# Kernel optimization log

Hardware: AMD Instinct MI355X
Metric: run time of the kernel (lower is better)

Reference implementation:

```python
import jax, jax.numpy as jnp
import numpy as np
import math

N = 4096      # nodes
E = 131072    # edges (avg degree 32)
C = 128       # input channels
RATIO = 0.5   # TopKPooling default ratio
DIMS = [(128, 256), (256, 512), (512, 512), (512, 256), (256, 128)]


def setup_inputs() -> dict:
    key = jax.random.key(0)
    ks = jax.random.split(key, 16)
    inp = {}
    inp['x'] = jax.random.normal(ks[0], (N, C), jnp.float32)
    inp['edge_index'] = jax.random.randint(ks[1], (2, E), 0, N, jnp.int32)
    for i, (fi, fo) in enumerate(DIMS):
        inp[f'w{i}'] = jax.random.normal(ks[2 + i], (fi, fo), jnp.float32) / np.sqrt(fi).astype(np.float32)
        inp[f'b{i}'] = jnp.zeros((fo,), jnp.float32)
    inp['p0'] = jax.random.normal(ks[10], (256,), jnp.float32)
    inp['p1'] = jax.random.normal(ks[11], (512,), jnp.float32)
    return inp


def _gcn(x, M, w, b):
    # GCNConv: add self loops (weight 1), symmetric D^-1/2 normalization with
    # deg computed over target (col) index, aggregate messages src->dst.
    # M[r, c] = weight of edge (src=r, dst=c); dense equivalent of sparse conv.
    n = M.shape[0]
    Mc = M + jnp.eye(n, dtype=M.dtype)
    deg = Mc.sum(axis=0)
    dis = jnp.where(deg > 0, jax.lax.rsqrt(deg), 0.0)
    A = dis[:, None] * Mc * dis[None, :]          # normalized (src, dst)
    return jax.nn.relu(A.T @ (x @ w) + b)          # out[dst] = sum_src A * xW


def _augment(M):
    # augment_adj: add self loops then spspmm(A, A) -> dense (M+I) @ (M+I)
    B = M + jnp.eye(M.shape[0], dtype=M.dtype)
    return B @ B


def _pool(x, M, p):
    # TopKPooling: score = tanh(x.p / ||p||), keep top ceil(ratio*n) nodes,
    # gate kept features by score, slice adjacency to kept nodes.
    s = jnp.tanh((x @ p) / jnp.linalg.norm(p))
    k = int(math.ceil(RATIO * x.shape[0]))
    vals, perm = jax.lax.top_k(s, k)
    return x[perm] * vals[:, None], M[perm][:, perm], perm


def reference(x, edge_index, w0, b0, w1, b1, w2, b2, w3, b3, w4, b4, p0, p1):
    # dense adjacency M[src, dst] from edge list with unit edge weights
    M = jnp.zeros((N, N), jnp.float32).at[edge_index[0], edge_index[1]].add(1.0)

    # down block 0
    x = _gcn(x, M, w0, b0)
    res0, M0 = x, M
    x, M, perm0 = _pool(x, _augment(M), p0)

    # down block 1
    x = _gcn(x, M, w1, b1)
    res1, M1 = x, M
    x, M, perm1 = _pool(x, _augment(M), p1)

    # bottleneck
    x = _gcn(x, M, w2, b2)

    # up block 1: scatter into zeros, sum residual
    up = jnp.zeros_like(res1).at[perm1].set(x)
    x = _gcn(res1 + up, M1, w3, b3)

    # up block 0
    up = jnp.zeros_like(res0).at[perm0].set(x)
    x = _gcn(res0 + up, M0, w4, b4)
    return x
```

## Files before the change

### kernel.cpp

```cpp
#include <hip/hip_runtime.h>

#define NN 4096
#define EE 131072
#define NP1 2048
#define NP2 1024

typedef __attribute__((ext_vector_type(8))) __bf16 bf16x8;
typedef __attribute__((ext_vector_type(4))) float f32x4;
typedef __attribute__((ext_vector_type(8))) unsigned short ushort8;

static __device__ inline unsigned short bfbits(__bf16 b) {
  union { __bf16 x; unsigned short u; } c; c.x = b; return c.u;
}
static __device__ inline void split2(float v, unsigned short& h, unsigned short& l) {
  __bf16 hb = (__bf16)v;
  float hf = (float)hb;
  __bf16 lb = (__bf16)(v - hf);
  h = bfbits(hb); l = bfbits(lb);
}

static __device__ inline size_t pchunk(int r, int k, int NT) {
  return ((size_t)(r >> 4) * NT + (k >> 5)) * 64 + (((k >> 3) & 3) << 4) + (r & 15);
}


__global__ void hist_kernel(const int* __restrict__ src, const int* __restrict__ dst,
                            int* __restrict__ cnt_src, int* __restrict__ cnt_dst, int E) {
  int e = blockIdx.x * blockDim.x + threadIdx.x;
  if (e < E) {
    atomicAdd(&cnt_src[src[e]], 1);
    atomicAdd(&cnt_dst[dst[e]], 1);
  }
}

__global__ __launch_bounds__(1024) void scan2(const int* __restrict__ cnt_dst,
                                              const int* __restrict__ cnt_src,
                                              int* __restrict__ csc_off, int* __restrict__ csr_off,
                                              float* __restrict__ dis0, int n) {
  __shared__ int tmp[4096];
  const int* in = blockIdx.x ? cnt_src : cnt_dst;
  int* out = blockIdx.x ? csr_off : csc_off;
  int tid = threadIdx.x;
  for (int i = tid; i < n; i += 1024) {
    int v = in[i];
    tmp[i] = v;
    if (blockIdx.x == 0) dis0[i] = rsqrtf((float)v + 1.0f);
  }
  __syncthreads();
  for (int off = 1; off < n; off <<= 1) {
    int v[4];
    int c = 0;
    for (int i = tid; i < n; i += 1024) { v[c++] = (i >= off) ? tmp[i - off] : 0; }
    __syncthreads();
    c = 0;
    for (int i = tid; i < n; i += 1024) { tmp[i] += v[c++]; }
    __syncthreads();
  }
  for (int i = tid; i < n; i += 1024) out[i + 1] = tmp[i];
  if (tid == 0) out[0] = 0;
}

__global__ void scatter_kernel(const int* __restrict__ src, const int* __restrict__ dst,
                               const int* __restrict__ csc_off, const int* __restrict__ csr_off,
                               int* __restrict__ fill_dst, int* __restrict__ fill_src,
                               int* __restrict__ csc_src, int* __restrict__ csr_dst, int E) {
  int e = blockIdx.x * blockDim.x + threadIdx.x;
  if (e < E) {
    int s = src[e], d = dst[e];
    int p = atomicAdd(&fill_dst[d], 1);
    csc_src[csc_off[d] + p] = s;
    int q = atomicAdd(&fill_src[s], 1);
    csr_dst[csr_off[s] + q] = d;
  }
}

__global__ void pnorm2(const float* __restrict__ p0, const float* __restrict__ p1,
                       float* __restrict__ outv) {
  const float* p = blockIdx.x ? p1 : p0;
  int C = blockIdx.x ? 512 : 256;
  int tid = threadIdx.x;
  float acc = 0.f;
  for (int j = tid; j < C; j += 256) { float v = p[j]; acc += v * v; }
  for (int o = 32; o > 0; o >>= 1) acc += __shfl_down(acc, o);
  __shared__ float red[4];
  if ((tid & 63) == 0) red[tid >> 6] = acc;
  __syncthreads();
  if (tid == 0) outv[blockIdx.x] = sqrtf(red[0] + red[1] + red[2] + red[3]);
}


__global__ void score_key(const float* __restrict__ X, const float* __restrict__ p,
                          const float* __restrict__ pn, float* __restrict__ s,
                          unsigned long long* __restrict__ keys, int C) {
  int i = blockIdx.x;
  int tid = threadIdx.x;
  float acc = 0.f;
  for (int j = tid; j < C; j += 256) acc += X[(size_t)i * C + j] * p[j];
  for (int o = 32; o > 0; o >>= 1) acc += __shfl_down(acc, o);
  __shared__ float red[4];
  if ((tid & 63) == 0) red[tid >> 6] = acc;
  __syncthreads();
  if (tid == 0) {
    float sv = tanhf((red[0] + red[1] + red[2] + red[3]) / pn[0]);
    s[i] = sv;
    unsigned u = __float_as_uint(sv);
    unsigned m = (u & 0x80000000u) ? ~u : (u | 0x80000000u);
    keys[i] = (((unsigned long long)(~m)) << 32) | (unsigned)i;
  }
}

__global__ __launch_bounds__(256) void rank_count(const unsigned long long* __restrict__ keys,
                                                  int* __restrict__ rank) {
  __shared__ unsigned long long kk[512];
  int tid = threadIdx.x;
  int cand = blockIdx.x * 256 + tid;
  int base = blockIdx.y * 512;
  kk[tid] = keys[base + tid];
  kk[tid + 256] = keys[base + tid + 256];
  __syncthreads();
  unsigned long long kc = keys[cand];
  int c = 0;
#pragma unroll 8
  for (int t = 0; t < 512; ++t) c += (kk[t] < kc) ? 1 : 0;
  atomicAdd(&rank[cand], c);
}

__global__ void rank_place(const float* __restrict__ s, const int* __restrict__ rank, int k, int n,
                           int* __restrict__ kept, int* __restrict__ perm, float* __restrict__ vals,
                           int* __restrict__ cntk) {
  int i = blockIdx.x * blockDim.x + threadIdx.x;
  if (i < n) {
    int r = rank[i];
    int isk = (r < k) ? 1 : 0;
    if (isk) { perm[r] = i; vals[r] = s[i]; kept[i] = r; }
    else kept[i] = -1;
    if (cntk) cntk[i] = isk;
  }
}

__global__ void pool_gather_s(const float* __restrict__ X, const int* __restrict__ perm,
                              const float* __restrict__ vals, const float* __restrict__ dis,
                              float* __restrict__ out, int C) {
  int a = blockIdx.x;
  int r = perm[a];
  float v = vals[a] * dis[a];
  for (int j = threadIdx.x; j < C; j += blockDim.x)
    out[(size_t)a * C + j] = X[(size_t)r * C + j] * v;
}

__global__ void pool_split_p(const float* __restrict__ X, const int* __restrict__ perm,
                             const float* __restrict__ vals, unsigned short* __restrict__ h,
                             unsigned short* __restrict__ l, int C) {
  int a = blockIdx.x;
  int r = perm[a];
  float v = vals[a];
  int NT = C >> 5;
  for (int j0 = threadIdx.x * 8; j0 < C; j0 += 64 * 8) {
    ushort8 hv, lv;
#pragma unroll
    for (int e = 0; e < 8; ++e) {
      unsigned short he, le;
      split2(X[(size_t)r * C + j0 + e] * v, he, le);
      hv[e] = he; lv[e] = le;
    }
    size_t c = pchunk(a, j0, NT);
    *(ushort8*)&h[c * 8] = hv;
    *(ushort8*)&l[c * 8] = lv;
  }
}


__global__ __launch_bounds__(256) void aug_row_p(const int* __restrict__ csr_off,
                                                 const int* __restrict__ csr_dst,
                                                 const int* __restrict__ kept,
                                                 const int* __restrict__ perm,
                                                 unsigned short* __restrict__ rm) {
  __shared__ float acc[NP1];
  int ki = blockIdx.x;
  int r = perm[ki];
  for (int t = threadIdx.x; t < NP1; t += 256) acc[t] = 0.f;
  __syncthreads();
  int s = csr_off[r], e = csr_off[r + 1];
  int nm = e - s;
  int wave = threadIdx.x >> 6, lane = threadIdx.x & 63;
  for (int m = wave; m <= nm; m += 4) {
    int k = (m < nm) ? csr_dst[s + m] : r;
    int s2 = csr_off[k], e2 = csr_off[k + 1];
    int n2 = e2 - s2;
    for (int t = lane; t <= n2; t += 64) {
      int j = (t < n2) ? csr_dst[s2 + t] : k;
      int kj = kept[j];
      if (kj >= 0) atomicAdd(&acc[kj], 1.0f);
    }
  }
  __syncthreads();
  if (threadIdx.x == 0) acc[ki] += 1.0f;
  __syncthreads();
  int tid = threadIdx.x;
  ushort8 hv;
#pragma unroll
  for (int e8 = 0; e8 < 8; ++e8) hv[e8] = bfbits((__bf16)acc[tid * 8 + e8]);
  size_t dst = (((size_t)(ki >> 4)) * 64 + (tid >> 2)) * 64 + (size_t)(tid & 3) * 16 + (ki & 15);
  *(ushort8*)&rm[dst * 8] = hv;
}

__global__ void cnt_edges(const int* __restrict__ src, const int* __restrict__ dst,
                          const int* __restrict__ kept, int* __restrict__ cntk, int E) {
  int e = blockIdx.x * blockDim.x + threadIdx.x;
  if (e < E && kept[src[e]] >= 0) atomicAdd(&cntk[dst[e]], 1);
}

__global__ __launch_bounds__(256) void deg_gather(const int* __restrict__ csc_off,
                                                  const int* __restrict__ csc_src,
                                                  const int* __restrict__ cntk,
                                                  const int* __restrict__ perm,
                                                  float* __restrict__ dis) {
  int wid = threadIdx.x >> 6, lane = threadIdx.x & 63;
  int c = blockIdx.x * 4 + wid;
  int r = perm[c];
  int s = csc_off[r], e = csc_off[r + 1];
  int sum = 0;
  for (int t = s + lane; t < e; t += 64) sum += cntk[csc_src[t]];
  for (int o = 32; o > 0; o >>= 1) sum += __shfl_down(sum, o);
  if (lane == 0) dis[c] = rsqrtf((float)(sum + cntk[r] + 1));
}

__global__ __launch_bounds__(256) void t_pack(const unsigned short* __restrict__ in,
                                              unsigned short* __restrict__ outp, int n) {
  __shared__ unsigned short t[64][72];
  int r0 = blockIdx.y * 64, c0 = blockIdx.x * 64;
  int NT = n >> 5;
  for (int q = threadIdx.x; q < 512; q += 256) {
    int lt = q >> 6, l = q & 63;
    int rt = lt >> 1, kt2 = lt & 1;
    int r = rt * 16 + (l & 15), k = kt2 * 32 + (l >> 4) * 8;
    ushort8 v = *(const ushort8*)&in[pchunk(r0 + r, c0 + k, NT) * 8];
    *(ushort8*)&t[r][k] = v;
  }
  __syncthreads();
  for (int q = threadIdx.x; q < 512; q += 256) {
    int lt = q >> 6, l = q & 63;
    int jt = lt >> 1, kt2 = lt & 1;
    int j = jt * 16 + (l & 15), k = kt2 * 32 + (l >> 4) * 8;
    ushort8 v;
#pragma unroll
    for (int e = 0; e < 8; ++e) v[e] = t[k + e][j];
    *(ushort8*)&outp[pchunk(c0 + j, r0 + k, NT) * 8] = v;
  }
}

__global__ void dis_from_deg(const float* __restrict__ deg, float* __restrict__ dis, int n) {
  int i = blockIdx.x * blockDim.x + threadIdx.x;
  if (i < n) dis[i] = rsqrtf(deg[i]);
}


__global__ void split_p(const float* __restrict__ in, unsigned short* __restrict__ h,
                        unsigned short* __restrict__ l, int K) {
  int c = blockIdx.x * blockDim.x + threadIdx.x;
  int lane = c & 63, tile = c >> 6;
  int NT = K >> 5;
  int kt = tile % NT, rt = tile / NT;
  int r = rt * 16 + (lane & 15);
  int k = kt * 32 + (lane >> 4) * 8;
  const float* p = in + (size_t)r * K + k;
  ushort8 hv, lv;
#pragma unroll
  for (int e = 0; e < 8; ++e) {
    unsigned short he, le;
    split2(p[e], he, le);
    hv[e] = he; lv[e] = le;
  }
  *(ushort8*)&h[(size_t)c * 8] = hv;
  *(ushort8*)&l[(size_t)c * 8] = lv;
}

static __device__ inline void tsplit_body(const float* in, unsigned short* oh, unsigned short* ol,
                                          int R, int C, int c) {
  int lane = c & 63, tile = c >> 6;
  int NT = R >> 5;
  int kt = tile % NT, jt = tile / NT;
  int j = jt * 16 + (lane & 15);
  int k = kt * 32 + (lane >> 4) * 8;
  ushort8 hv, lv;
#pragma unroll
  for (int e = 0; e < 8; ++e) {
    unsigned short he, le;
    split2(in[(size_t)(k + e) * C + j], he, le);
    hv[e] = he; lv[e] = le;
  }
  *(ushort8*)&oh[(size_t)c * 8] = hv;
  *(ushort8*)&ol[(size_t)c * 8] = lv;
}

__global__ void tsplit_p(const float* __restrict__ in, unsigned short* __restrict__ oh,
                         unsigned short* __restrict__ ol, int R, int C) {
  int c = blockIdx.x * blockDim.x + threadIdx.x;
  tsplit_body(in, oh, ol, R, C, c);
}

__global__ void wconv_all(const float* w0, const float* w1, const float* w2,
                          const float* w3, const float* w4,
                          unsigned short* o0h, unsigned short* o0l,
                          unsigned short* o1h, unsigned short* o1l,
                          unsigned short* o2h, unsigned short* o2l,
                          unsigned short* o3h, unsigned short* o3l,
                          unsigned short* o4h, unsigned short* o4l) {
  int g = blockIdx.x * blockDim.x + threadIdx.x;
  if (g < 4096)        tsplit_body(w0, o0h, o0l, 128, 256, g);
  else if (g < 20480)  tsplit_body(w1, o1h, o1l, 256, 512, g - 4096);
  else if (g < 53248)  tsplit_body(w2, o2h, o2l, 512, 512, g - 20480);
  else if (g < 69632)  tsplit_body(w3, o3h, o3l, 512, 256, g - 53248);
  else                 tsplit_body(w4, o4h, o4l, 256, 128, g - 69632);
}

__global__ void gather2_p(const unsigned short* __restrict__ in0, const unsigned short* __restrict__ in1,
                          const int* __restrict__ perm,
                          unsigned short* __restrict__ out0, unsigned short* __restrict__ out1, int NT) {
  const unsigned short* in = blockIdx.y ? in1 : in0;
  unsigned short* outp = blockIdx.y ? out1 : out0;
  int c = blockIdx.x * blockDim.x + threadIdx.x;
  int lane = c & 63, tile = c >> 6;
  int kt = tile % NT, at = tile / NT;
  int a = at * 16 + (lane & 15);
  int sub = lane >> 4;
  int p = perm[a];
  size_t sc = ((size_t)(p >> 4) * NT + kt) * 64 + sub * 16 + (p & 15);
  *(ushort8*)&outp[(size_t)c * 8] = *(const ushort8*)&in[sc * 8];
}

__global__ void unpool_split_p(const float* __restrict__ res, const float* __restrict__ up,
                               const int* __restrict__ kept, unsigned short* __restrict__ h,
                               unsigned short* __restrict__ l, int C) {
  int c = blockIdx.x * blockDim.x + threadIdx.x;
  int lane = c & 63, tile = c >> 6;
  int NT = C >> 5;
  int kt = tile % NT, rt = tile / NT;
  int r = rt * 16 + (lane & 15);
  int j0 = kt * 32 + (lane >> 4) * 8;
  int kv = kept[r];
  ushort8 hv, lv;
#pragma unroll
  for (int e = 0; e < 8; ++e) {
    float v = res[(size_t)r * C + j0 + e];
    if (kv >= 0) v += up[(size_t)kv * C + j0 + e];
    unsigned short he, le;
// ... 31 lines not shown
  float* o = out + (size_t)c * C + j;
#pragma unroll
  for (int u = 0; u < VEC; ++u) o[u] = dc * acc[u];
}

template <int C>
__global__ __launch_bounds__(256) void spmm_gather_v(const float* __restrict__ Y,
                                                     const int* __restrict__ off,
                                                     const int* __restrict__ srcs,
                                                     const float* __restrict__ dis,
                                                     const float* __restrict__ bias,
                                                     float* __restrict__ out) {
  constexpr int VEC = C / 64;
  int w = threadIdx.x >> 6, lane = threadIdx.x & 63;
  int c = blockIdx.x * 4 + w;
  int j = lane * VEC;
  float acc[VEC];
  const float* p = Y + (size_t)c * C + j;
#pragma unroll
  for (int u = 0; u < VEC; ++u) acc[u] = p[u];
  int s = off[c], e = off[c + 1];
  for (int t = s; t < e; ++t) {
    const float* q = Y + (size_t)srcs[t] * C + j;
#pragma unroll
    for (int u = 0; u < VEC; ++u) acc[u] += q[u];
  }
  float d = dis[c];
  float* o = out + (size_t)c * C + j;
#pragma unroll
  for (int u = 0; u < VEC; ++u) o[u] = fmaxf(d * acc[u] + bias[j + u], 0.0f);
}


template <int S>
__global__ void ep3(const float* __restrict__ p, const float* __restrict__ rs,
                    const float* __restrict__ bias, float* __restrict__ outp, int M, int N) {
  int idx = blockIdx.x * blockDim.x + threadIdx.x;
  int j4 = (idx * 4) % N, i = (idx * 4) / N;
  float4 a = {0.f, 0.f, 0.f, 0.f};
#pragma unroll
  for (int s = 0; s < S; ++s) {
    float4 b = *(const float4*)(p + ((size_t)s * M + i) * N + j4);
    a.x += b.x; a.y += b.y; a.z += b.z; a.w += b.w;
  }
  float r = rs[i];
  float4 o;
  o.x = fmaxf(r * a.x + bias[j4 + 0], 0.f);
  o.y = fmaxf(r * a.y + bias[j4 + 1], 0.f);
  o.z = fmaxf(r * a.z + bias[j4 + 2], 0.f);
  o.w = fmaxf(r * a.w + bias[j4 + 3], 0.f);
  *(float4*)(outp + (size_t)i * N + j4) = o;
}

template <int S>
__global__ void ep_zsplit(const float* __restrict__ p, unsigned short* __restrict__ h,
                          unsigned short* __restrict__ l, int M, int N) {
  int t = blockIdx.x * blockDim.x + threadIdx.x;
  int tile = t >> 6, w = t & 63;
  int NT = N >> 5;
  int rt = tile / NT, kt = tile % NT;
  int r = rt * 16 + (w & 15);
  int k = kt * 32 + (w >> 4) * 8;
  const float* p0 = p + (size_t)r * N + k;
  ushort8 hv, lv;
#pragma unroll
  for (int e = 0; e < 8; ++e) {
    float v = p0[e];
#pragma unroll
    for (int s = 1; s < S; ++s) v += p0[(size_t)s * M * N + e];
    unsigned short he, le;
    split2(v, he, le);
    hv[e] = he; lv[e] = le;
  }
  *(ushort8*)&h[(size_t)t * 8] = hv;
  *(ushort8*)&l[(size_t)t * 8] = lv;
}

template <int S>
__global__ void ep_aug_cs(const float* __restrict__ p, float* __restrict__ B,
                          float* __restrict__ deg, int n) {
  int c = blockIdx.x * 256 + threadIdx.x;
  int r0 = blockIdx.y * 64;
  float cs = 0.f;
  for (int r = r0; r < r0 + 64; ++r) {
    float v = 0.f;
#pragma unroll
    for (int s = 0; s < S; ++s) v += p[((size_t)s * n + r) * n + c];
    if (r == c) v += 1.0f;
    B[(size_t)r * n + c] = v;
    cs += v;
  }
  atomicAdd(&deg[c], cs);
}

template <int EPI, int AL, int BL, int KK, int S>
__global__ __launch_bounds__(256) void gemm16(
    const unsigned short* __restrict__ Ah, const unsigned short* __restrict__ Al,
    const unsigned short* __restrict__ Bh, const unsigned short* __restrict__ Bl,
    int M, int N, const float* __restrict__ rs, const float* __restrict__ bias,
    float* __restrict__ C, unsigned short* __restrict__ Th, unsigned short* __restrict__ Tl) {
  static_assert(KK % 32 == 0, "K");
  constexpr int KSTEPS = KK / 32;
  const int NT = (KK * S) >> 5;
  const int gx = gridDim.x;
  int id = blockIdx.y * gx + blockIdx.x;
  int cpx = (gx * gridDim.y) >> 3;
  int sid = (id & 7) * cpx + (id >> 3);
  const int bx = sid % gx, by = sid / gx;
  const int z = (S > 1) ? blockIdx.z : 0;
  const int wid = threadIdx.x >> 6, lane = threadIdx.x & 63;
  const int i0 = by * 64 + (wid >> 1) * 32;
  const int j0 = bx * 64 + (wid & 1) * 32;
  const int lr = lane & 15, lk = lane >> 4;
  size_t aoff[2], boff[2];
#pragma unroll
  for (int t = 0; t < 2; ++t) {
    aoff[t] = ((size_t)((i0 >> 4) + t) * NT + z * (KK >> 5)) * 512 + lane * 8;
    boff[t] = ((size_t)((j0 >> 4) + t) * NT + z * (KK >> 5)) * 512 + lane * 8;
  }
  const f32x4 zf = {0.f, 0.f, 0.f, 0.f};
  f32x4 acc[2][2];
  acc[0][0] = zf; acc[0][1] = zf; acc[1][0] = zf; acc[1][1] = zf;

  bf16x8 ahf[4][2], bhf[4][2], alf[4][2], blf[4][2];
  auto loadk = [&](int kk, int b) {
    size_t o = (size_t)kk * 512;
    ahf[b][0] = *(const bf16x8*)(Ah + aoff[0] + o);
    ahf[b][1] = *(const bf16x8*)(Ah + aoff[1] + o);
// ... 16 lines not shown
        acc[am][bn] = __builtin_amdgcn_mfma_f32_16x16x32_bf16(ahf[b][am], bhf[b][bn], acc[am][bn], 0, 0, 0);
        if constexpr (BL)
          acc[am][bn] = __builtin_amdgcn_mfma_f32_16x16x32_bf16(ahf[b][am], blf[b][bn], acc[am][bn], 0, 0, 0);
        if constexpr (AL)
          acc[am][bn] = __builtin_amdgcn_mfma_f32_16x16x32_bf16(alf[b][am], bhf[b][bn], acc[am][bn], 0, 0, 0);
      }
  };

  loadk(0, 0);
  if constexpr (KSTEPS > 1) loadk(1, 1);
  if constexpr (KSTEPS > 2) loadk(2, 2);
#pragma unroll
  for (int kk = 0; kk < KSTEPS; ++kk) {
    const int cur = kk & 3;
    if (kk + 3 < KSTEPS) loadk(kk + 3, (cur + 3) & 3);
    domm(cur);
  }

#pragma unroll
  for (int am = 0; am < 2; ++am)
#pragma unroll
    for (int bn = 0; bn < 2; ++bn) {
      int ib = i0 + 16 * am + lk * 4;
      int j = j0 + 16 * bn + lr;
      f32x4 a = acc[am][bn];
      if constexpr (S > 1) {
#pragma unroll
        for (int r = 0; r < 4; ++r) C[((size_t)z * M + ib + r) * N + j] = a[r];
      } else if constexpr (EPI == 0) {
#pragma unroll
        for (int r = 0; r < 4; ++r) C[(size_t)(ib + r) * N + j] = a[r];
      } else if constexpr (EPI == 1) {
#pragma unroll
        for (int r = 0; r < 4; ++r) C[(size_t)(ib + r) * N + j] = rs[ib + r] * a[r];
      } else if constexpr (EPI == 2) {
        unsigned long long hp = 0, lp = 0;
#pragma unroll
        for (int r = 0; r < 4; ++r) {
          unsigned short hv, lv;
          split2(rs[ib + r] * a[r], hv, lv);
          hp |= ((unsigned long long)hv) << (16 * r);
          lp |= ((unsigned long long)lv) << (16 * r);
        }
        size_t c = pchunk(j, ib, M >> 5);
        *(unsigned long long*)&Th[c * 8 + (ib & 7)] = hp;
        *(unsigned long long*)&Tl[c * 8 + (ib & 7)] = lp;
      } else if constexpr (EPI == 3) {
#pragma unroll
        for (int r = 0; r < 4; ++r)
          C[(size_t)(ib + r) * N + j] = fmaxf(rs[ib + r] * a[r] + bias[j], 0.0f);
      } else {
#pragma unroll
        for (int r = 0; r < 4; ++r)
          C[(size_t)(ib + r) * N + j] = fmaxf(a[r] + bias[j], 0.0f);
      }
    }
}

template <int AL, int BL, int KK, int S>
__global__ __launch_bounds__(256) void gemm64(
    const unsigned short* __restrict__ Ah, const unsigned short* __restrict__ Al,
    const unsigned short* __restrict__ Bh, const unsigned short* __restrict__ Bl,
    int M, int N, float* __restrict__ C) {
  static_assert(KK % 32 == 0, "K");
  constexpr int KSTEPS = KK / 32;
  const int NT = (KK * S) >> 5;
  const int gx = gridDim.x;
  int id = blockIdx.y * gx + blockIdx.x;
  int cpx = (gx * gridDim.y) >> 3;
  int sid = (id & 7) * cpx + (id >> 3);
  const int bx = sid % gx, by = sid / gx;
  const int z = blockIdx.z;
  const int wid = threadIdx.x >> 6, lane = threadIdx.x & 63;
  const int i0 = by * 128 + (wid >> 1) * 64;
  const int j0 = bx * 128 + (wid & 1) * 64;
  const int lr = lane & 15, lk = lane >> 4;
  size_t aoff[4], boff[4];
#pragma unroll
  for (int t = 0; t < 4; ++t) {
    aoff[t] = ((size_t)((i0 >> 4) + t) * NT + z * (KK >> 5)) * 512 + lane * 8;
    boff[t] = ((size_t)((j0 >> 4) + t) * NT + z * (KK >> 5)) * 512 + lane * 8;
  }
  const f32x4 zf = {0.f, 0.f, 0.f, 0.f};
// ... 66 lines not shown
  const float* b3 = (const float*)d_in[9];
  const float* w4 = (const float*)d_in[10];
  const float* b4 = (const float*)d_in[11];
  const float* p0 = (const float*)d_in[12];
  const float* p1 = (const float*)d_in[13];
  float* out = (float*)d_out;

  char* ws = (char*)d_ws;
  size_t off = 0;
  auto alloc = [&](size_t b) { void* p = ws + off; off += (b + 255) & ~(size_t)255; return p; };

  int* csc_off = (int*)alloc(4 * (NN + 1));
  int* csr_off = (int*)alloc(4 * (NN + 1));
  int* csc_src = (int*)alloc(4 * EE);
  int* csr_dst = (int*)alloc(4 * EE);

  size_t zero_bytes = 4 * NN * 4 + 4 * NP2 + 4 * NN + 4 * NP1;
  int* cnts    = (int*)alloc(zero_bytes);
  int* cnt_dst = cnts;
  int* cnt_src = cnts + NN;
  int* fill_dst = cnts + 2 * NN;
  int* fill_src = cnts + 3 * NN;
  float* deg2 = (float*)(cnts + 4 * NN);
  int* rank0 = (int*)(deg2 + NP2);
  int* rank1 = rank0 + NN;

  int* cntk  = (int*)alloc(4 * NN);
  int* kept0 = (int*)alloc(4 * NN);
  int* perm0 = (int*)alloc(4 * NP1);
  int* kept1 = (int*)alloc(4 * NP1);
  int* perm1 = (int*)alloc(4 * NP2);
  float* dis0 = (float*)alloc(4 * NN);
  float* dis1 = (float*)alloc(4 * NP1);
  float* dis2 = (float*)alloc(4 * NP2);
  float* pnrm = (float*)alloc(8);
  float* s0   = (float*)alloc(4 * NN);
  float* vals0 = (float*)alloc(4 * NP1);
  float* s1   = (float*)alloc(4 * NP1);
  float* vals1 = (float*)alloc(4 * NP2);
  unsigned long long* keys0 = (unsigned long long*)alloc(8 * NN);
  unsigned long long* keys1 = (unsigned long long*)alloc(8 * NP1);

  const size_t MB = 1024 * 1024;
  char* regB1 = (char*)alloc(16 * MB);
  unsigned short* Gh2 = (unsigned short*)regB1;
  unsigned short* Hh2 = (unsigned short*)(regB1 + 4 * MB);
  float* B2   = (float*)regB1;
  unsigned short* B2th = (unsigned short*)(regB1 + 4 * MB);
  unsigned short* B2tl = (unsigned short*)(regB1 + 6 * MB);
  float* pscr = (float*)alloc(16 * MB);

  unsigned short* B1rm = (unsigned short*)alloc(8 * MB);
  unsigned short* B1t  = (unsigned short*)alloc(8 * MB);
  float* res0 = (float*)alloc(4 * MB);
  float* res1 = (float*)alloc(4 * MB);
  float* yreg = (float*)alloc(4 * MB);
  float* Gspmm = yreg;
  float* outreg = (float*)alloc(2 * MB);
  float* x1s = outreg;
  float* out2 = outreg, *out3 = outreg;
  char* ytreg = (char*)alloc(4 * MB);
  unsigned short* Y2th = (unsigned short*)ytreg;
  unsigned short* Y2tl = (unsigned short*)(ytreg + 1 * MB);
  unsigned short* Y3th = (unsigned short*)ytreg;
  unsigned short* Y3tl = (unsigned short*)(ytreg + 1 * MB);
  char* xsreg = (char*)alloc(4 * MB);
  unsigned short* x3h = (unsigned short*)xsreg;
  unsigned short* x3l = (unsigned short*)(xsreg + 2 * MB);
  unsigned short* x4h = (unsigned short*)xsreg;
  unsigned short* x4l = (unsigned short*)(xsreg + 2 * MB);
  unsigned short* xh = (unsigned short*)alloc(1 * MB);
  unsigned short* xl = (unsigned short*)alloc(1 * MB);
  char* xsm = (char*)alloc(2 * MB);
  unsigned short* x1th = (unsigned short*)xsm;
  unsigned short* x1tl = (unsigned short*)(xsm + 1 * MB);
  unsigned short* Zh = (unsigned short*)xsm;
  unsigned short* Zl = (unsigned short*)(xsm + 1 * MB);
  unsigned short* x2h = (unsigned short*)xsm;
  unsigned short* x2l = (unsigned short*)(xsm + 1 * MB);
  unsigned short* Wt0h = (unsigned short*)alloc(256 * 128 * 2);
  unsigned short* Wt0l = (unsigned short*)alloc(256 * 128 * 2);
  unsigned short* Wt1h = (unsigned short*)alloc(512 * 256 * 2);
  unsigned short* Wt1l = (unsigned short*)alloc(512 * 256 * 2);
  unsigned short* Wt2h = (unsigned short*)alloc(512 * 512 * 2);
  unsigned short* Wt2l = (unsigned short*)alloc(512 * 512 * 2);
  unsigned short* Wt3h = (unsigned short*)alloc(256 * 512 * 2);
  unsigned short* Wt3l = (unsigned short*)alloc(256 * 512 * 2);
  unsigned short* Wt4h = (unsigned short*)alloc(128 * 256 * 2);
  unsigned short* Wt4l = (unsigned short*)alloc(128 * 256 * 2);

  hipMemsetAsync(cnts, 0, zero_bytes, stream);

  hist_kernel<<<EE / 256, 256, 0, stream>>>(esrc, edst, cnt_src, cnt_dst, EE);
  scan2<<<2, 1024, 0, stream>>>(cnt_dst, cnt_src, csc_off, csr_off, dis0, NN);
  scatter_kernel<<<EE / 256, 256, 0, stream>>>(esrc, edst, csc_off, csr_off,
                                               fill_dst, fill_src, csc_src, csr_dst, EE);
  pnorm2<<<2, 256, 0, stream>>>(p0, p1, pnrm);
  wconv_all<<<288, 256, 0, stream>>>(w0, w1, w2, w3, w4, Wt0h, Wt0l, Wt1h, Wt1l,
                                     Wt2h, Wt2l, Wt3h, Wt3l, Wt4h, Wt4l);

  spmm_pre<128><<<NN / 4, 256, 0, stream>>>(x, csc_off, csc_src, dis0, Gspmm);
  split_p<<<(NN * 128 / 8) / 256, 256, 0, stream>>>(Gspmm, xh, xl, 128);
  gemm16<4, 1, 1, 128, 1><<<dim3(4, 64), 256, 0, stream>>>(xh, xl, Wt0h, Wt0l,
                                                           NN, 256, nullptr, b0, res0, nullptr, nullptr);

  score_key<<<NN, 256, 0, stream>>>(res0, p0, pnrm + 0, s0, keys0, 256);
  rank_count<<<dim3(NN / 256, NN / 512), 256, 0, stream>>>(keys0, rank0);
  rank_place<<<NN / 256, 256, 0, stream>>>(s0, rank0, NP1, NN, kept0, perm0, vals0, cntk);

  aug_row_p<<<NP1, 256, 0, stream>>>(csr_off, csr_dst, kept0, perm0, B1rm);
  cnt_edges<<<EE / 256, 256, 0, stream>>>(esrc, edst, kept0, cntk, EE);
  deg_gather<<<NP1 / 4, 256, 0, stream>>>(csc_off, csc_src, cntk, perm0, dis1);
  t_pack<<<dim3(32, 32), 256, 0, stream>>>(B1rm, B1t, NP1);

  pool_gather_s<<<NP1, 256, 0, stream>>>(res0, perm0, vals0, dis1, x1s, 256);
  tsplit_p<<<(NP1 * 256 / 8) / 256, 256, 0, stream>>>(x1s, x1th, x1tl, NP1, 256);
  gemm16<0, 0, 1, 1024, 2><<<dim3(4, 32, 2), 256, 0, stream>>>(B1t, nullptr, x1th, x1tl,
                                                               NP1, 256, nullptr, nullptr, pscr, nullptr, nullptr);
  ep_zsplit<2><<<(NP1 * 256 / 8) / 256, 256, 0, stream>>>(pscr, Zh, Zl, NP1, 256);
  gemm16<3, 1, 1, 256, 1><<<dim3(8, 32), 256, 0, stream>>>(Zh, Zl, Wt1h, Wt1l,
                                                           NP1, 512, dis1, b1, res1, nullptr, nullptr);

  score_key<<<NP1, 256, 0, stream>>>(res1, p1, pnrm + 1, s1, keys1, 512);
  rank_count<<<dim3(NP1 / 256, NP1 / 512), 256, 0, stream>>>(keys1, rank1);
  rank_place<<<NP1 / 256, 256, 0, stream>>>(s1, rank1, NP2, NP1, kept1, perm1, vals1, nullptr);
  pool_split_p<<<NP2, 64, 0, stream>>>(res1, perm1, vals1, x2h, x2l, 512);

  gather2_p<<<dim3((NP2 * NP1 / 8) / 256, 2), 256, 0, stream>>>(B1rm, B1t, perm1, Gh2, Hh2, NP1 >> 5);
  gemm64<0, 0, 512, 4><<<dim3(8, 8, 4), 256, 0, stream>>>(Gh2, nullptr, Hh2, nullptr,
                                                          NP2, NP2, pscr);
  ep_aug_cs<4><<<dim3(NP2 / 256, NP2 / 64), 256, 0, stream>>>(pscr, B2, deg2, NP2);
  dis_from_deg<<<NP2 / 256, 256, 0, stream>>>(deg2, dis2, NP2);
  tsplit_p<<<(NP2 * NP2 / 8) / 256, 256, 0, stream>>>(B2, B2th, B2tl, NP2, NP2);

  gemm16<2, 1, 1, 512, 1><<<dim3(8, 16), 256, 0, stream>>>(x2h, x2l, Wt2h, Wt2l,
                                                           NP2, 512, dis2, nullptr, nullptr, Y2th, Y2tl);
  gemm16<0, 1, 1, 512, 2><<<dim3(8, 16, 2), 256, 0, stream>>>(B2th, B2tl, Y2th, Y2tl,
                                                              NP2, 512, nullptr, nullptr, pscr, nullptr, nullptr);
  ep3<2><<<(NP2 * 512) / 1024, 256, 0, stream>>>(pscr, dis2, b2, out2, NP2, 512);

  unpool_split_p<<<(NP1 * 512 / 8) / 256, 256, 0, stream>>>(res1, out2, kept1, x3h, x3l, 512);
  gemm16<2, 1, 1, 512, 1><<<dim3(4, 32), 256, 0, stream>>>(x3h, x3l, Wt3h, Wt3l,
                                                           NP1, 256, dis1, nullptr, nullptr, Y3th, Y3tl);
  gemm64<0, 1, 256, 8><<<dim3(2, 16, 8), 256, 0, stream>>>(B1t, nullptr, Y3th, Y3tl,
                                                           NP1, 256, pscr);
  ep3<8><<<(NP1 * 256) / 1024, 256, 0, stream>>>(pscr, dis1, b3, out3, NP1, 256);

  unpool_split_p<<<(NN * 256 / 8) / 256, 256, 0, stream>>>(res0, out3, kept0, x4h, x4l, 256);
  gemm16<1, 1, 1, 256, 1><<<dim3(2, 64), 256, 0, stream>>>(x4h, x4l, Wt4h, Wt4l,
                                                           NN, 128, dis0, nullptr, yreg, nullptr, nullptr);
  spmm_gather_v<128><<<NN / 4, 256, 0, stream>>>(yreg, csc_off, csc_src, dis0, b4, out);
}
```

Before: 339.8 us.

## Fuse small prep and pooling kernels to cut launches and intermediate buffers

Merges the edge histogram, weight transpose-split and p-norm kernels into one launch, and merges the augmented-row build with kept-edge counting. It also merges the B1 transpose with the degree gather, and fuses pool gather with the transpose-split. The augment epilogue now writes the split transposed bf16 B2 directly, and the GEMM and ep3 epilogues compute rsqrt of deg2 inline, which removes the fp32 B2 round trip, dis_from_deg and a tsplit pass. The aim is fewer kernel launches and less global memory traffic. In exchange, the merged kernels mix heterogeneous block types, which can cause load imbalance.

```diff
diff --git a/kernel.cpp b/kernel.cpp
--- a/kernel.cpp
+++ b/kernel.cpp
@@ -23,13 +23,57 @@
   return ((size_t)(r >> 4) * NT + (k >> 5)) * 64 + (((k >> 3) & 3) << 4) + (r & 15);
 }
 
-
-__global__ void hist_kernel(const int* __restrict__ src, const int* __restrict__ dst,
-                            int* __restrict__ cnt_src, int* __restrict__ cnt_dst, int E) {
-  int e = blockIdx.x * blockDim.x + threadIdx.x;
-  if (e < E) {
-    atomicAdd(&cnt_src[src[e]], 1);
-    atomicAdd(&cnt_dst[dst[e]], 1);
+static __device__ inline void tsplit_body(const float* in, unsigned short* oh, unsigned short* ol,
+                                          int R, int C, int c) {
+  int lane = c & 63, tile = c >> 6;
+  int NT = R >> 5;
+  int kt = tile % NT, jt = tile / NT;
+  int j = jt * 16 + (lane & 15);
+  int k = kt * 32 + (lane >> 4) * 8;
+  ushort8 hv, lv;
+#pragma unroll
+  for (int e = 0; e < 8; ++e) {
+    unsigned short he, le;
+    split2(in[(size_t)(k + e) * C + j], he, le);
+    hv[e] = he; lv[e] = le;
+  }
+  *(ushort8*)&oh[(size_t)c * 8] = hv;
+  *(ushort8*)&ol[(size_t)c * 8] = lv;
+}
+
+
+__global__ __launch_bounds__(256) void prep_all(
+    const int* __restrict__ esrc, const int* __restrict__ edst,
+    int* __restrict__ cnt_src, int* __restrict__ cnt_dst,
+    const float* w0, const float* w1, const float* w2, const float* w3, const float* w4,
+    unsigned short* o0h, unsigned short* o0l, unsigned short* o1h, unsigned short* o1l,
+    unsigned short* o2h, unsigned short* o2l, unsigned short* o3h, unsigned short* o3l,
+    unsigned short* o4h, unsigned short* o4l,
+    const float* p0, const float* p1, float* pnrm) {
+  __shared__ float red[4];
+  int b = blockIdx.x;
+  int tid = threadIdx.x;
+  if (b < EE / 256) {
+    int e = b * 256 + tid;
+    atomicAdd(&cnt_src[esrc[e]], 1);
+    atomicAdd(&cnt_dst[edst[e]], 1);
+  } else if (b < EE / 256 + 288) {
+    int g = (b - EE / 256) * 256 + tid;
+    if (g < 4096)        tsplit_body(w0, o0h, o0l, 128, 256, g);
+    else if (g < 20480)  tsplit_body(w1, o1h, o1l, 256, 512, g - 4096);
+    else if (g < 53248)  tsplit_body(w2, o2h, o2l, 512, 512, g - 20480);
+    else if (g < 69632)  tsplit_body(w3, o3h, o3l, 512, 256, g - 53248);
+    else                 tsplit_body(w4, o4h, o4l, 256, 128, g - 69632);
+  } else {
+    int which = b - (EE / 256 + 288);
+    const float* p = which ? p1 : p0;
+    int C = which ? 512 : 256;
+    float acc = 0.f;
+    for (int j = tid; j < C; j += 256) { float v = p[j]; acc += v * v; }
+    for (int o = 32; o > 0; o >>= 1) acc += __shfl_down(acc, o);
+    if ((tid & 63) == 0) red[tid >> 6] = acc;
+    __syncthreads();
+    if (tid == 0) pnrm[which] = sqrtf(red[0] + red[1] + red[2] + red[3]);
   }
 }
 
@@ -72,20 +116,6 @@
     int q = atomicAdd(&fill_src[s], 1);
     csr_dst[csr_off[s] + q] = d;
   }
-}
-
-__global__ void pnorm2(const float* __restrict__ p0, const float* __restrict__ p1,
-                       float* __restrict__ outv) {
-  const float* p = blockIdx.x ? p1 : p0;
-  int C = blockIdx.x ? 512 : 256;
-  int tid = threadIdx.x;
-  float acc = 0.f;
-  for (int j = tid; j < C; j += 256) { float v = p[j]; acc += v * v; }
-  for (int o = 32; o > 0; o >>= 1) acc += __shfl_down(acc, o);
-  __shared__ float red[4];
-  if ((tid & 63) == 0) red[tid >> 6] = acc;
-  __syncthreads();
-  if (tid == 0) outv[blockIdx.x] = sqrtf(red[0] + red[1] + red[2] + red[3]);
 }
 
 
@@ -138,16 +168,6 @@
   }
 }
 
-__global__ void pool_gather_s(const float* __restrict__ X, const int* __restrict__ perm,
-                              const float* __restrict__ vals, const float* __restrict__ dis,
-                              float* __restrict__ out, int C) {
-  int a = blockIdx.x;
-  int r = perm[a];
-  float v = vals[a] * dis[a];
-  for (int j = threadIdx.x; j < C; j += blockDim.x)
-    out[(size_t)a * C + j] = X[(size_t)r * C + j] * v;
-}
-
 __global__ void pool_split_p(const float* __restrict__ X, const int* __restrict__ perm,
                              const float* __restrict__ vals, unsigned short* __restrict__ h,
                              unsigned short* __restrict__ l, int C) {
@@ -169,89 +189,112 @@
   }
 }
 
-
-__global__ __launch_bounds__(256) void aug_row_p(const int* __restrict__ csr_off,
-                                                 const int* __restrict__ csr_dst,
-                                                 const int* __restrict__ kept,
-                                                 const int* __restrict__ perm,
-                                                 unsigned short* __restrict__ rm) {
+__global__ void pool_tsplit_p(const float* __restrict__ X, const int* __restrict__ perm,
+                              const float* __restrict__ vals, const float* __restrict__ dis,
+                              unsigned short* __restrict__ h, unsigned short* __restrict__ l) {
+  int c = blockIdx.x * blockDim.x + threadIdx.x;
+  int tile = c >> 6, lno = c & 63;
+  int kt = tile & 63, jt = tile >> 6;
+  int j = jt * 16 + (lno & 15);
+  int k0 = kt * 32 + (lno >> 4) * 8;
+  ushort8 hv, lv;
+#pragma unroll
+  for (int e = 0; e < 8; ++e) {
+    int node = k0 + e;
+    float sc = vals[node] * dis[node];
+    float v = X[(size_t)perm[node] * 256 + j] * sc;
+    unsigned short he, le;
+    split2(v, he, le);
+    hv[e] = he; lv[e] = le;
+  }
+  *(ushort8*)&h[(size_t)c * 8] = hv;
+  *(ushort8*)&l[(size_t)c * 8] = lv;
+}
+
+
+__global__ __launch_bounds__(256) void augcnt(const int* __restrict__ csr_off,
+                                              const int* __restrict__ csr_dst,
+                                              const int* __restrict__ kept,
+                                              const int* __restrict__ perm,
+                                              unsigned short* __restrict__ rm,
+                                              const int* __restrict__ esrc,
+                                              const int* __restrict__ edst,
+                                              int* __restrict__ cntk) {
   __shared__ float acc[NP1];
-  int ki = blockIdx.x;
-  int r = perm[ki];
-  for (int t = threadIdx.x; t < NP1; t += 256) acc[t] = 0.f;
-  __syncthreads();
-  int s = csr_off[r], e = csr_off[r + 1];
-  int nm = e - s;
-  int wave = threadIdx.x >> 6, lane = threadIdx.x & 63;
-  for (int m = wave; m <= nm; m += 4) {
-    int k = (m < nm) ? csr_dst[s + m] : r;
-    int s2 = csr_off[k], e2 = csr_off[k + 1];
-    int n2 = e2 - s2;
-    for (int t = lane; t <= n2; t += 64) {
-      int j = (t < n2) ? csr_dst[s2 + t] : k;
-      int kj = kept[j];
-      if (kj >= 0) atomicAdd(&acc[kj], 1.0f);
-    }
-  }
-  __syncthreads();
-  if (threadIdx.x == 0) acc[ki] += 1.0f;
-  __syncthreads();
-  int tid = threadIdx.x;
-  ushort8 hv;
-#pragma unroll
-  for (int e8 = 0; e8 < 8; ++e8) hv[e8] = bfbits((__bf16)acc[tid * 8 + e8]);
-  size_t dst = (((size_t)(ki >> 4)) * 64 + (tid >> 2)) * 64 + (size_t)(tid & 3) * 16 + (ki & 15);
-  *(ushort8*)&rm[dst * 8] = hv;
-}
-
-__global__ void cnt_edges(const int* __restrict__ src, const int* __restrict__ dst,
-                          const int* __restrict__ kept, int* __restrict__ cntk, int E) {
-  int e = blockIdx.x * blockDim.x + threadIdx.x;
-  if (e < E && kept[src[e]] >= 0) atomicAdd(&cntk[dst[e]], 1);
-}
-
-__global__ __launch_bounds__(256) void deg_gather(const int* __restrict__ csc_off,
-                                                  const int* __restrict__ csc_src,
-                                                  const int* __restrict__ cntk,
-                                                  const int* __restrict__ perm,
-                                                  float* __restrict__ dis) {
-  int wid = threadIdx.x >> 6, lane = threadIdx.x & 63;
-  int c = blockIdx.x * 4 + wid;
-  int r = perm[c];
-  int s = csc_off[r], e = csc_off[r + 1];
-  int sum = 0;
-  for (int t = s + lane; t < e; t += 64) sum += cntk[csc_src[t]];
-  for (int o = 32; o > 0; o >>= 1) sum += __shfl_down(sum, o);
-  if (lane == 0) dis[c] = rsqrtf((float)(sum + cntk[r] + 1));
-}
-
-__global__ __launch_bounds__(256) void t_pack(const unsigned short* __restrict__ in,
-                                              unsigned short* __restrict__ outp, int n) {
+  int b = blockIdx.x;
+  if (b < NP1) {
+    int ki = b;
+    int r = perm[ki];
+    for (int t = threadIdx.x; t < NP1; t += 256) acc[t] = 0.f;
+    __syncthreads();
+    int s = csr_off[r], e = csr_off[r + 1];
+    int nm = e - s;
+    int wave = threadIdx.x >> 6, lane = threadIdx.x & 63;
+    for (int m = wave; m <= nm; m += 4) {
+      int k = (m < nm) ? csr_dst[s + m] : r;
+      int s2 = csr_off[k], e2 = csr_off[k + 1];
+      int n2 = e2 - s2;
+      for (int t = lane; t <= n2; t += 64) {
+        int j = (t < n2) ? csr_dst[s2 + t] : k;
+        int kj = kept[j];
+        if (kj >= 0) atomicAdd(&acc[kj], 1.0f);
+      }
+    }
+    __syncthreads();
+    if (threadIdx.x == 0) acc[ki] += 1.0f;
+    __syncthreads();
+    int tid = threadIdx.x;
+    ushort8 hv;
+#pragma unroll
+    for (int e8 = 0; e8 < 8; ++e8) hv[e8] = bfbits((__bf16)acc[tid * 8 + e8]);
+    size_t dst = (((size_t)(ki >> 4)) * 64 + (tid >> 2)) * 64 + (size_t)(tid & 3) * 16 + (ki & 15);
+    *(ushort8*)&rm[dst * 8] = hv;
+  } else {
+    int e = (b - NP1) * 256 + threadIdx.x;
+    if (kept[esrc[e]] >= 0) atomicAdd(&cntk[edst[e]], 1);
+  }
+}
+
+__global__ __launch_bounds__(256) void degtp(const unsigned short* __restrict__ in,
+                                             unsigned short* __restrict__ outp, int n,
+                                             const int* __restrict__ csc_off,
+                                             const int* __restrict__ csc_src,
+                                             const int* __restrict__ cntk,
+                                             const int* __restrict__ perm,
+                                             float* __restrict__ dis) {
   __shared__ unsigned short t[64][72];
-  int r0 = blockIdx.y * 64, c0 = blockIdx.x * 64;
-  int NT = n >> 5;
-  for (int q = threadIdx.x; q < 512; q += 256) {
-    int lt = q >> 6, l = q & 63;
-    int rt = lt >> 1, kt2 = lt & 1;
-    int r = rt * 16 + (l & 15), k = kt2 * 32 + (l >> 4) * 8;
-    ushort8 v = *(const ushort8*)&in[pchunk(r0 + r, c0 + k, NT) * 8];
-    *(ushort8*)&t[r][k] = v;
-  }
-  __syncthreads();
-  for (int q = threadIdx.x; q < 512; q += 256) {
-    int lt = q >> 6, l = q & 63;
-    int jt = lt >> 1, kt2 = lt & 1;
-    int j = jt * 16 + (l & 15), k = kt2 * 32 + (l >> 4) * 8;
-    ushort8 v;
-#pragma unroll
-    for (int e = 0; e < 8; ++e) v[e] = t[k + e][j];
-    *(ushort8*)&outp[pchunk(c0 + j, r0 + k, NT) * 8] = v;
-  }
-}
-
-__global__ void dis_from_deg(const float* __restrict__ deg, float* __restrict__ dis, int n) {
-  int i = blockIdx.x * blockDim.x + threadIdx.x;
-  if (i < n) dis[i] = rsqrtf(deg[i]);
+  int b = blockIdx.x;
+  if (b < 1024) {
+    int r0 = (b >> 5) * 64, c0 = (b & 31) * 64;
+    int NT = n >> 5;
+    for (int q = threadIdx.x; q < 512; q += 256) {
+      int lt = q >> 6, l = q & 63;
+      int rt = lt >> 1, kt2 = lt & 1;
+      int r = rt * 16 + (l & 15), k = kt2 * 32 + (l >> 4) * 8;
+      ushort8 v = *(const ushort8*)&in[pchunk(r0 + r, c0 + k, NT) * 8];
+      *(ushort8*)&t[r][k] = v;
+    }
+    __syncthreads();
+    for (int q = threadIdx.x; q < 512; q += 256) {
+      int lt = q >> 6, l = q & 63;
+      int jt = lt >> 1, kt2 = lt & 1;
+      int j = jt * 16 + (l & 15), k = kt2 * 32 + (l >> 4) * 8;
+      ushort8 v;
+#pragma unroll
+      for (int e = 0; e < 8; ++e) v[e] = t[k + e][j];
+      *(ushort8*)&outp[pchunk(c0 + j, r0 + k, NT) * 8] = v;
+    }
+  } else {
+    int bid = b - 1024;
+    int wid = threadIdx.x >> 6, lane = threadIdx.x & 63;
+    int c = bid * 4 + wid;
+    int r = perm[c];
+    int s = csc_off[r], e = csc_off[r + 1];
+    int sum = 0;
+    for (int t2 = s + lane; t2 < e; t2 += 64) sum += cntk[csc_src[t2]];
+    for (int o = 32; o > 0; o >>= 1) sum += __shfl_down(sum, o);
+    if (lane == 0) dis[c] = rsqrtf((float)(sum + cntk[r] + 1));
+  }
 }
 
 
@@ -273,45 +316,6 @@
   }
   *(ushort8*)&h[(size_t)c * 8] = hv;
   *(ushort8*)&l[(size_t)c * 8] = lv;
-}
-
-static __device__ inline void tsplit_body(const float* in, unsigned short* oh, unsigned short* ol,
-                                          int R, int C, int c) {
-  int lane = c & 63, tile = c >> 6;
-  int NT = R >> 5;
-  int kt = tile % NT, jt = tile / NT;
-  int j = jt * 16 + (lane & 15);
-  int k = kt * 32 + (lane >> 4) * 8;
-  ushort8 hv, lv;
-#pragma unroll
-  for (int e = 0; e < 8; ++e) {
-    unsigned short he, le;
-    split2(in[(size_t)(k + e) * C + j], he, le);
-    hv[e] = he; lv[e] = le;
-  }
-  *(ushort8*)&oh[(size_t)c * 8] = hv;
-  *(ushort8*)&ol[(size_t)c * 8] = lv;
-}
-
-__global__ void tsplit_p(const float* __restrict__ in, unsigned short* __restrict__ oh,
-                         unsigned short* __restrict__ ol, int R, int C) {
-  int c = blockIdx.x * blockDim.x + threadIdx.x;
-  tsplit_body(in, oh, ol, R, C, c);
-}
-
-__global__ void wconv_all(const float* w0, const float* w1, const float* w2,
-                          const float* w3, const float* w4,
-                          unsigned short* o0h, unsigned short* o0l,
-                          unsigned short* o1h, unsigned short* o1l,
-                          unsigned short* o2h, unsigned short* o2l,
-                          unsigned short* o3h, unsigned short* o3l,
-                          unsigned short* o4h, unsigned short* o4l) {
-  int g = blockIdx.x * blockDim.x + threadIdx.x;
-  if (g < 4096)        tsplit_body(w0, o0h, o0l, 128, 256, g);
-  else if (g < 20480)  tsplit_body(w1, o1h, o1l, 256, 512, g - 4096);
-  else if (g < 53248)  tsplit_body(w2, o2h, o2l, 512, 512, g - 20480);
-  else if (g < 69632)  tsplit_body(w3, o3h, o3l, 512, 256, g - 53248);
-  else                 tsplit_body(w4, o4h, o4l, 256, 128, g - 69632);
 }
 
 __global__ void gather2_p(const unsigned short* __restrict__ in0, const unsigned short* __restrict__ in1,
@@ -409,7 +413,7 @@
 }
 
 
-template <int S>
+template <int S, int RSQ>
 __global__ void ep3(const float* __restrict__ p, const float* __restrict__ rs,
                     const float* __restrict__ bias, float* __restrict__ outp, int M, int N) {
   int idx = blockIdx.x * blockDim.x + threadIdx.x;
@@ -421,6 +425,7 @@
     a.x += b.x; a.y += b.y; a.z += b.z; a.w += b.w;
   }
   float r = rs[i];
+  if (RSQ) r = rsqrtf(r);
   float4 o;
   o.x = fmaxf(r * a.x + bias[j4 + 0], 0.f);
   o.y = fmaxf(r * a.y + bias[j4 + 1], 0.f);
@@ -454,23 +459,39 @@
 }
 
 template <int S>
-__global__ void ep_aug_cs(const float* __restrict__ p, float* __restrict__ B,
-                          float* __restrict__ deg, int n) {
+__global__ void ep_aug_cs2(const float* __restrict__ p, unsigned short* __restrict__ th,
+                           unsigned short* __restrict__ tl, float* __restrict__ deg, int n) {
   int c = blockIdx.x * 256 + threadIdx.x;
   int r0 = blockIdx.y * 64;
+  int NT = n >> 5;
   float cs = 0.f;
-  for (int r = r0; r < r0 + 64; ++r) {
-    float v = 0.f;
-#pragma unroll
-    for (int s = 0; s < S; ++s) v += p[((size_t)s * n + r) * n + c];
-    if (r == c) v += 1.0f;
-    B[(size_t)r * n + c] = v;
-    cs += v;
+  for (int g = 0; g < 8; ++g) {
+    float vbuf[8];
+#pragma unroll
+    for (int e = 0; e < 8; ++e) {
+      int r = r0 + g * 8 + e;
+      float v = 0.f;
+#pragma unroll
+      for (int s = 0; s < S; ++s) v += p[((size_t)s * n + r) * n + c];
+      if (r == c) v += 1.0f;
+      vbuf[e] = v;
+      cs += v;
+    }
+    ushort8 hv, lv;
+#pragma unroll
+    for (int e = 0; e < 8; ++e) {
+      unsigned short he, le;
+      split2(vbuf[e], he, le);
+      hv[e] = he; lv[e] = le;
+    }
+    size_t ch = pchunk(c, r0 + g * 8, NT);
+    *(ushort8*)&th[ch * 8] = hv;
+    *(ushort8*)&tl[ch * 8] = lv;
   }
   atomicAdd(&deg[c], cs);
 }
 
-template <int EPI, int AL, int BL, int KK, int S>
+template <int EPI, int AL, int BL, int KK, int S, int RSQ>
 __global__ __launch_bounds__(256) void gemm16(
     const unsigned short* __restrict__ Ah, const unsigned short* __restrict__ Al,
     const unsigned short* __restrict__ Bh, const unsigned short* __restrict__ Bl,
@@ -553,13 +574,19 @@
         for (int r = 0; r < 4; ++r) C[(size_t)(ib + r) * N + j] = a[r];
       } else if constexpr (EPI == 1) {
 #pragma unroll
-        for (int r = 0; r < 4; ++r) C[(size_t)(ib + r) * N + j] = rs[ib + r] * a[r];
+        for (int r = 0; r < 4; ++r) {
+          float rsv = rs[ib + r];
+          if (RSQ) rsv = rsqrtf(rsv);
+          C[(size_t)(ib + r) * N + j] = rsv * a[r];
+        }
       } else if constexpr (EPI == 2) {
         unsigned long long hp = 0, lp = 0;
 #pragma unroll
         for (int r = 0; r < 4; ++r) {
+          float rsv = rs[ib + r];
+          if (RSQ) rsv = rsqrtf(rsv);
           unsigned short hv, lv;
-          split2(rs[ib + r] * a[r], hv, lv);
+          split2(rsv * a[r], hv, lv);
           hp |= ((unsigned long long)hv) << (16 * r);
           lp |= ((unsigned long long)lv) << (16 * r);
         }
@@ -568,8 +595,11 @@
         *(unsigned long long*)&Tl[c * 8 + (ib & 7)] = lp;
       } else if constexpr (EPI == 3) {
 #pragma unroll
-        for (int r = 0; r < 4; ++r)
-          C[(size_t)(ib + r) * N + j] = fmaxf(rs[ib + r] * a[r] + bias[j], 0.0f);
+        for (int r = 0; r < 4; ++r) {
+          float rsv = rs[ib + r];
+          if (RSQ) rsv = rsqrtf(rsv);
+          C[(size_t)(ib + r) * N + j] = fmaxf(rsv * a[r] + bias[j], 0.0f);
+        }
       } else {
 #pragma unroll
         for (int r = 0; r < 4; ++r)
@@ -702,7 +732,6 @@
   int* perm1 = (int*)alloc(4 * NP2);
   float* dis0 = (float*)alloc(4 * NN);
   float* dis1 = (float*)alloc(4 * NP1);
-  float* dis2 = (float*)alloc(4 * NP2);
   float* pnrm = (float*)alloc(8);
   float* s0   = (float*)alloc(4 * NN);
   float* vals0 = (float*)alloc(4 * NP1);
@@ -715,7 +744,6 @@
   char* regB1 = (char*)alloc(16 * MB);
   unsigned short* Gh2 = (unsigned short*)regB1;
   unsigned short* Hh2 = (unsigned short*)(regB1 + 4 * MB);
-  float* B2   = (float*)regB1;
   unsigned short* B2th = (unsigned short*)(regB1 + 4 * MB);
   unsigned short* B2tl = (unsigned short*)(regB1 + 6 * MB);
   float* pscr = (float*)alloc(16 * MB);
@@ -727,7 +755,6 @@
   float* yreg = (float*)alloc(4 * MB);
   float* Gspmm = yreg;
   float* outreg = (float*)alloc(2 * MB);
-  float* x1s = outreg;
   float* out2 = outreg, *out3 = outreg;
   char* ytreg = (char*)alloc(4 * MB);
   unsigned short* Y2th = (unsigned short*)ytreg;
@@ -761,35 +788,32 @@
 
   hipMemsetAsync(cnts, 0, zero_bytes, stream);
 
-  hist_kernel<<<EE / 256, 256, 0, stream>>>(esrc, edst, cnt_src, cnt_dst, EE);
+  prep_all<<<EE / 256 + 288 + 2, 256, 0, stream>>>(
+      esrc, edst, cnt_src, cnt_dst, w0, w1, w2, w3, w4,
+      Wt0h, Wt0l, Wt1h, Wt1l, Wt2h, Wt2l, Wt3h, Wt3l, Wt4h, Wt4l, p0, p1, pnrm);
   scan2<<<2, 1024, 0, stream>>>(cnt_dst, cnt_src, csc_off, csr_off, dis0, NN);
   scatter_kernel<<<EE / 256, 256, 0, stream>>>(esrc, edst, csc_off, csr_off,
                                                fill_dst, fill_src, csc_src, csr_dst, EE);
-  pnorm2<<<2, 256, 0, stream>>>(p0, p1, pnrm);
-  wconv_all<<<288, 256, 0, stream>>>(w0, w1, w2, w3, w4, Wt0h, Wt0l, Wt1h, Wt1l,
-                                     Wt2h, Wt2l, Wt3h, Wt3l, Wt4h, Wt4l);
 
   spmm_pre<128><<<NN / 4, 256, 0, stream>>>(x, csc_off, csc_src, dis0, Gspmm);
   split_p<<<(NN * 128 / 8) / 256, 256, 0, stream>>>(Gspmm, xh, xl, 128);
-  gemm16<4, 1, 1, 128, 1><<<dim3(4, 64), 256, 0, stream>>>(xh, xl, Wt0h, Wt0l,
-                                                           NN, 256, nullptr, b0, res0, nullptr, nullptr);
+  gemm16<4, 1, 1, 128, 1, 0><<<dim3(4, 64), 256, 0, stream>>>(xh, xl, Wt0h, Wt0l,
+                                                              NN, 256, nullptr, b0, res0, nullptr, nullptr);
 
   score_key<<<NN, 256, 0, stream>>>(res0, p0, pnrm + 0, s0, keys0, 256);
   rank_count<<<dim3(NN / 256, NN / 512), 256, 0, stream>>>(keys0, rank0);
   rank_place<<<NN / 256, 256, 0, stream>>>(s0, rank0, NP1, NN, kept0, perm0, vals0, cntk);
 
-  aug_row_p<<<NP1, 256, 0, stream>>>(csr_off, csr_dst, kept0, perm0, B1rm);
-  cnt_edges<<<EE / 256, 256, 0, stream>>>(esrc, edst, kept0, cntk, EE);
-  deg_gather<<<NP1 / 4, 256, 0, stream>>>(csc_off, csc_src, cntk, perm0, dis1);
-  t_pack<<<dim3(32, 32), 256, 0, stream>>>(B1rm, B1t, NP1);
-
-  pool_gather_s<<<NP1, 256, 0, stream>>>(res0, perm0, vals0, dis1, x1s, 256);
-  tsplit_p<<<(NP1 * 256 / 8) / 256, 256, 0, stream>>>(x1s, x1th, x1tl, NP1, 256);
-  gemm16<0, 0, 1, 1024, 2><<<dim3(4, 32, 2), 256, 0, stream>>>(B1t, nullptr, x1th, x1tl,
-                                                               NP1, 256, nullptr, nullptr, pscr, nullptr, nullptr);
+  augcnt<<<NP1 + EE / 256, 256, 0, stream>>>(csr_off, csr_dst, kept0, perm0, B1rm,
+                                             esrc, edst, cntk);
+  degtp<<<1024 + NP1 / 4, 256, 0, stream>>>(B1rm, B1t, NP1, csc_off, csc_src, cntk, perm0, dis1);
+
+  pool_tsplit_p<<<(NP1 * 256 / 8) / 256, 256, 0, stream>>>(res0, perm0, vals0, dis1, x1th, x1tl);
+  gemm16<0, 0, 1, 1024, 2, 0><<<dim3(4, 32, 2), 256, 0, stream>>>(B1t, nullptr, x1th, x1tl,
+                                                                  NP1, 256, nullptr, nullptr, pscr, nullptr, nullptr);
   ep_zsplit<2><<<(NP1 * 256 / 8) / 256, 256, 0, stream>>>(pscr, Zh, Zl, NP1, 256);
-  gemm16<3, 1, 1, 256, 1><<<dim3(8, 32), 256, 0, stream>>>(Zh, Zl, Wt1h, Wt1l,
-                                                           NP1, 512, dis1, b1, res1, nullptr, nullptr);
+  gemm16<3, 1, 1, 256, 1, 0><<<dim3(8, 32), 256, 0, stream>>>(Zh, Zl, Wt1h, Wt1l,
+                                                              NP1, 512, dis1, b1, res1, nullptr, nullptr);
 
   score_key<<<NP1, 256, 0, stream>>>(res1, p1, pnrm + 1, s1, keys1, 512);
   rank_count<<<dim3(NP1 / 256, NP1 / 512), 256, 0, stream>>>(keys1, rank1);
@@ -799,25 +823,23 @@
   gather2_p<<<dim3((NP2 * NP1 / 8) / 256, 2), 256, 0, stream>>>(B1rm, B1t, perm1, Gh2, Hh2, NP1 >> 5);
   gemm64<0, 0, 512, 4><<<dim3(8, 8, 4), 256, 0, stream>>>(Gh2, nullptr, Hh2, nullptr,
                                                           NP2, NP2, pscr);
-  ep_aug_cs<4><<<dim3(NP2 / 256, NP2 / 64), 256, 0, stream>>>(pscr, B2, deg2, NP2);
-  dis_from_deg<<<NP2 / 256, 256, 0, stream>>>(deg2, dis2, NP2);
-  tsplit_p<<<(NP2 * NP2 / 8) / 256, 256, 0, stream>>>(B2, B2th, B2tl, NP2, NP2);
-
-  gemm16<2, 1, 1, 512, 1><<<dim3(8, 16), 256, 0, stream>>>(x2h, x2l, Wt2h, Wt2l,
-                                                           NP2, 512, dis2, nullptr, nullptr, Y2th, Y2tl);
-  gemm16<0, 1, 1, 512, 2><<<dim3(8, 16, 2), 256, 0, stream>>>(B2th, B2tl, Y2th, Y2tl,
-                                                              NP2, 512, nullptr, nullptr, pscr, nullptr, nullptr);
-  ep3<2><<<(NP2 * 512) / 1024, 256, 0, stream>>>(pscr, dis2, b2, out2, NP2, 512);
+  ep_aug_cs2<4><<<dim3(NP2 / 256, NP2 / 64), 256, 0, stream>>>(pscr, B2th, B2tl, deg2, NP2);
+
+  gemm16<2, 1, 1, 512, 1, 1><<<dim3(8, 16), 256, 0, stream>>>(x2h, x2l, Wt2h, Wt2l,
+                                                              NP2, 512, deg2, nullptr, nullptr, Y2th, Y2tl);
+  gemm16<0, 1, 1, 512, 2, 0><<<dim3(8, 16, 2), 256, 0, stream>>>(B2th, B2tl, Y2th, Y2tl,
+                                                                 NP2, 512, nullptr, nullptr, pscr, nullptr, nullptr);
+  ep3<2, 1><<<(NP2 * 512) / 1024, 256, 0, stream>>>(pscr, deg2, b2, out2, NP2, 512);
 
   unpool_split_p<<<(NP1 * 512 / 8) / 256, 256, 0, stream>>>(res1, out2, kept1, x3h, x3l, 512);
-  gemm16<2, 1, 1, 512, 1><<<dim3(4, 32), 256, 0, stream>>>(x3h, x3l, Wt3h, Wt3l,
-                                                           NP1, 256, dis1, nullptr, nullptr, Y3th, Y3tl);
+  gemm16<2, 1, 1, 512, 1, 0><<<dim3(4, 32), 256, 0, stream>>>(x3h, x3l, Wt3h, Wt3l,
+                                                              NP1, 256, dis1, nullptr, nullptr, Y3th, Y3tl);
   gemm64<0, 1, 256, 8><<<dim3(2, 16, 8), 256, 0, stream>>>(B1t, nullptr, Y3th, Y3tl,
                                                            NP1, 256, pscr);
-  ep3<8><<<(NP1 * 256) / 1024, 256, 0, stream>>>(pscr, dis1, b3, out3, NP1, 256);
+  ep3<8, 0><<<(NP1 * 256) / 1024, 256, 0, stream>>>(pscr, dis1, b3, out3, NP1, 256);
 
   unpool_split_p<<<(NN * 256 / 8) / 256, 256, 0, stream>>>(res0, out3, kept0, x4h, x4l, 256);
-  gemm16<1, 1, 1, 256, 1><<<dim3(2, 64), 256, 0, stream>>>(x4h, x4l, Wt4h, Wt4l,
-                                                           NN, 128, dis0, nullptr, yreg, nullptr, nullptr);
+  gemm16<1, 1, 1, 256, 1, 0><<<dim3(2, 64), 256, 0, stream>>>(x4h, x4l, Wt4h, Wt4l,
+                                                              NN, 128, dis0, nullptr, yreg, nullptr, nullptr);
   spmm_gather_v<128><<<NN / 4, 256, 0, stream>>>(yreg, csc_off, csc_src, dis0, b4, out);
 }
```

Result: faster. 312.1 us (-8.2%).
